# Optimization experiments

Hardware: AMD Instinct MI355X
Metric: run time of the kernel (lower is better)

The kernel has to match this reference:

```python
import jax, jax.numpy as jnp
import numpy as np
import math

DK = 768  # latent_size used for the scale (not the per-head dim, matching the original)

def setup_inputs() -> dict:
    key = jax.random.key(0)
    k1, k2, k3 = jax.random.split(key, 3)
    B, H, S, D = 4, 12, 2048, 64
    queries = jax.random.normal(k1, (B, H, S, D), dtype=jnp.float32)
    keys = jax.random.normal(k2, (B, H, S, D), dtype=jnp.float32)
    values = jax.random.normal(k3, (B, S, H, D), dtype=jnp.float32)  # note [B,S,H,D] layout
    return {"queries": queries, "keys": keys, "values": values}

def reference(queries, keys, values):
    # scores: [B,H,S,S]
    scores = jnp.einsum('bhqd,bhkd->bhqk', queries, keys) / math.sqrt(DK)
    probs = jax.nn.softmax(scores, axis=3)
    v = jnp.transpose(values, (0, 2, 1, 3))  # [B,S,H,D] -> [B,H,S,D]
    return jnp.einsum('bhqk,bhkd->bhqd', probs, v)
```

## Files before the change

### kernel.cpp

```cpp
#include <hip/hip_runtime.h>

#define SQ 2048
#define DH 64
#define NH 12
#define NBH 48
#define QTILE 128
#define KTILE 64
#define NITER (SQ / KTILE)
#define NQT (SQ / QTILE)

typedef short short8 __attribute__((ext_vector_type(8)));
typedef float f32x4  __attribute__((ext_vector_type(4)));
typedef float f32x16 __attribute__((ext_vector_type(16)));
typedef int   i32x4 __attribute__((ext_vector_type(4)));

#define MFMA32(a, b, c) __builtin_amdgcn_mfma_f32_32x32x16_bf16(a, b, c, 0, 0, 0)

typedef __attribute__((address_space(1))) const void* gas_ptr;
typedef __attribute__((address_space(3))) void* las_ptr;

__device__ __forceinline__ void load_lds16(const void* g, void* l) {
    __builtin_amdgcn_global_load_lds((gas_ptr)g, (las_ptr)l, 16, 0, 0);
}

#if defined(__has_builtin) && __has_builtin(__builtin_amdgcn_cvt_pk_bf16_f32)
typedef __bf16 bf16x2_t __attribute__((ext_vector_type(2)));
__device__ __forceinline__ unsigned pk2bf(float a, float b) {
    bf16x2_t v = __builtin_amdgcn_cvt_pk_bf16_f32(a, b);
    union { bf16x2_t v; unsigned u; } c; c.v = v; return c.u;
}
#else
__device__ __forceinline__ unsigned pk2bf(float a, float b) {
    union { float f; unsigned u; } x, y; x.f = a; y.f = b;
    unsigned ra = x.u + 0x7FFFu + ((x.u >> 16) & 1u);
    unsigned rb = y.u + 0x7FFFu + ((y.u >> 16) & 1u);
    return (ra >> 16) | (rb & 0xFFFF0000u);
}
#endif

#define KCONV_BLOCKS (NBH * SQ * DH / 8 / 256)
__global__ __launch_bounds__(256)
void prepass(const float* __restrict__ K, short* __restrict__ Kb,
             const float* __restrict__ V, short* __restrict__ Vt) {
    __shared__ float Ls[64][68];
    if (blockIdx.x < KCONV_BLOCKS) {
        const size_t i = (size_t)(blockIdx.x * 256 + threadIdx.x) * 8;
        f32x4 a = *(const f32x4*)&K[i];
        f32x4 b = *(const f32x4*)&K[i + 4];
        unsigned o[4] = { pk2bf(a[0], a[1]), pk2bf(a[2], a[3]),
                          pk2bf(b[0], b[1]), pk2bf(b[2], b[3]) };
        *(i32x4*)&Kb[i] = *(i32x4*)o;
        return;
    }
    const int bx = blockIdx.x - KCONV_BLOCKS;
    const int st = bx & 31;
    const int bh = bx >> 5;
    const int b = bh / NH, h = bh % NH;
    const int s0 = st * 64;
    const float* src = V + ((size_t)b * SQ * NH + (size_t)h) * DH;
    const int dg = threadIdx.x & 15;
    const int sl = threadIdx.x >> 4;
    #pragma unroll
    for (int p = 0; p < 4; ++p) {
        const int row = p * 16 + sl;
        *(f32x4*)&Ls[row][dg * 4] =
            *(const f32x4*)&src[(size_t)(s0 + row) * (NH * DH) + dg * 4];
    }
    __syncthreads();
    const int dr = threadIdx.x >> 2;
    const int sc = (threadIdx.x & 3) * 16;
    unsigned out[8];
    #pragma unroll
    for (int jj = 0; jj < 8; ++jj)
        out[jj] = pk2bf(Ls[sc + 2 * jj][dr], Ls[sc + 2 * jj + 1][dr]);
    short* dst = Vt + (size_t)bh * DH * SQ + (size_t)dr * SQ + s0 + sc;
    *(i32x4*)(dst)     = *(i32x4*)&out[0];
    *(i32x4*)(dst + 8) = *(i32x4*)&out[4];
}

__global__ __launch_bounds__(256, 3)
void attn_fused_kernel(const float* __restrict__ Q,
                       const short* __restrict__ Kb,
                       const short* __restrict__ Vtg,
                       float* __restrict__ O) {
    __shared__ __align__(16) char L[32768];

    const int tid  = threadIdx.x;
    const int lane = tid & 63;
    const int w    = tid >> 6;
    const int m31  = lane & 31;
    const int hl   = lane >> 5;
    const int l7   = lane & 7;

    const int bx  = blockIdx.x;
    const int xcd = bx & 7;
    const int i96 = bx >> 3;
    const int bh  = xcd * 6 + (i96 % 6);
    const int qt  = i96 / 6;
    const int q0 = qt * QTILE;

    const float* Qb  = Q   + (size_t)bh * SQ * DH;
    const short* Kbh = Kb  + (size_t)bh * SQ * DH;
    const short* Vbh = Vtg + (size_t)bh * DH * SQ;
    float*       Ob  = O   + (size_t)bh * SQ * DH;

    const float qscale = 0.03608439182435161f * 1.4426950408889634f;

    short8 qf[4];
    {
        const int qrow = q0 + 32 * w + m31;
        #pragma unroll
        for (int s = 0; s < 4; ++s) {
            const float* src = Qb + (size_t)qrow * DH + 16 * s + 8 * hl;
            f32x4 qa = *(const f32x4*)src;
            f32x4 qb = *(const f32x4*)(src + 4);
            union { unsigned u[4]; short8 v; } f;
            f.u[0] = pk2bf(qa[0] * qscale, qa[1] * qscale);
            f.u[1] = pk2bf(qa[2] * qscale, qa[3] * qscale);
            f.u[2] = pk2bf(qb[0] * qscale, qb[1] * qscale);
            f.u[3] = pk2bf(qb[2] * qscale, qb[3] * qscale);
            qf[s] = f.v;
        }
    }

    const int gk = (lane & 7) ^ (lane >> 3);
    const int rr = w * 8 + (lane >> 3);
    const short* kg0 = Kbh + (size_t)rr * DH + gk * 8;
    const short* kg1 = kg0 + 32 * DH;
    const short* vg0 = Vbh + (size_t)rr * SQ + gk * 8;
    const short* vg1 = vg0 + 32 * SQ;
    const int wslot = w * 1024;

    int aoff[4];
    #pragma unroll
    for (int s = 0; s < 4; ++s) aoff[s] = m31 * 128 + (((2 * s + hl) ^ l7) * 16);

    f32x16 o0 = {}, o1 = {};
    float lp = 0.f;

    auto issue = [&](int bb) {
        load_lds16(kg0, L + bb + wslot);
        load_lds16(kg1, L + bb + 4096 + wslot);
        load_lds16(vg0, L + bb + 8192 + wslot);
        load_lds16(vg1, L + bb + 12288 + wslot);
        kg0 += KTILE * DH; kg1 += KTILE * DH;
        vg0 += KTILE;      vg1 += KTILE;
    };

    auto softmax_pack = [&](const f32x16& sv, short8* dst) {
        #pragma unroll
        for (int wd = 0; wd < 2; ++wd) {
            float p[8];
            #pragma unroll
            for (int j = 0; j < 8; ++j)
                p[j] = __builtin_amdgcn_exp2f(sv[8 * wd + j]);
            lp += ((p[0] + p[1]) + (p[2] + p[3])) +
                  ((p[4] + p[5]) + (p[6] + p[7]));
            unsigned a0 = pk2bf(p[0], p[1]);
            unsigned a1 = pk2bf(p[2], p[3]);
            unsigned b0 = pk2bf(p[4], p[5]);
            unsigned b1 = pk2bf(p[6], p[7]);
            unsigned r0 = (unsigned)__shfl_xor((int)(hl ? a0 : b0), 32, 64);
            unsigned r1 = (unsigned)__shfl_xor((int)(hl ? a1 : b1), 32, 64);
            union { unsigned u[4]; short8 v; } fr;
            fr.u[0] = hl ? r0 : a0;
            fr.u[1] = hl ? r1 : a1;
            fr.u[2] = hl ? b0 : r0;
            fr.u[3] = hl ? b1 : r1;
            dst[wd] = fr.v;
        }
    };

    auto compute = [&](int bb) {
        f32x16 s0 = {}, s1 = {};
        #pragma unroll
        for (int s = 0; s < 4; ++s) {
            short8 ka0 = *(const short8*)(L + bb + aoff[s]);
            short8 ka1 = *(const short8*)(L + bb + 4096 + aoff[s]);
            s0 = MFMA32(ka0, qf[s], s0);
            s1 = MFMA32(ka1, qf[s], s1);
        }
        short8 pfrag[4];
        softmax_pack(s0, &pfrag[0]);
        softmax_pack(s1, &pfrag[2]);
        #pragma unroll
        for (int s = 0; s < 4; ++s) {
            short8 vb0 = *(const short8*)(L + bb + 8192 + aoff[s]);
            short8 vb1 = *(const short8*)(L + bb + 12288 + aoff[s]);
            o0 = MFMA32(pfrag[s], vb0, o0);
            o1 = MFMA32(pfrag[s], vb1, o1);
        }
    };

    issue(0);
    for (int it = 0; it < NITER; it += 2) {
        __syncthreads();
        issue(16384);
        compute(0);
        __syncthreads();
        if (it + 2 < NITER) issue(0);
        compute(16384);
    }

    float v = lp;
    v += __shfl_xor(v, 32, 64);
    const float linv = 1.0f / v;

    #pragma unroll
    for (int dt = 0; dt < 2; ++dt) {
        const f32x16& o = dt ? o1 : o0;
        #pragma unroll
        for (int reg = 0; reg < 16; ++reg) {
            const int qp = (reg & 3) + 8 * (reg >> 2) + 4 * hl;
            const float rl = __shfl(linv, qp, 64);
            const int q = q0 + 32 * w + qp;
            Ob[(size_t)q * DH + 32 * dt + m31] = o[reg] * rl;
        }
    }
}

extern "C" void kernel_launch(void* const* d_in, const int* in_sizes, int n_in,
                              void* d_out, int out_size, void* d_ws, size_t ws_size,
                              hipStream_t stream) {
    const float* Q = (const float*)d_in[0];
    const float* K = (const float*)d_in[1];
    const float* V = (const float*)d_in[2];
    float* O = (float*)d_out;

    short* Kb  = (short*)d_ws;
    short* Vtg = Kb + (size_t)NBH * SQ * DH;

    prepass<<<dim3(KCONV_BLOCKS + NBH * 32), dim3(256), 0, stream>>>(K, Kb, V, Vtg);
    attn_fused_kernel<<<dim3(NBH * NQT), dim3(256), 0, stream>>>(Q, Kb, Vtg, O);
}
```

Measured before the change: 175.6 us.

## Software-pipeline QK of next tile with softmax and PV of current tile

K and V now get separate double-buffered LDS slots and are issued on their own schedules. The main loop computes QK scores for tile t+1 while running exp/pack and the PV MFMAs for tile t, with one barrier per tile instead of one per half-step. This lets the MFMA work overlap the transcendental softmax work. The cross-half shuffle is replaced by permlane32_swap when the builtin exists, and the row sum is accumulated as a packed float2. The cost is extra registers to hold the next tile's scores, which may reduce occupancy at launch bounds of 3 blocks.

```diff
diff --git a/kernel.cpp b/kernel.cpp
--- a/kernel.cpp
+++ b/kernel.cpp
@@ -10,8 +10,10 @@
 #define NQT (SQ / QTILE)
 
 typedef short short8 __attribute__((ext_vector_type(8)));
+typedef float f32x2  __attribute__((ext_vector_type(2)));
 typedef float f32x4  __attribute__((ext_vector_type(4)));
 typedef float f32x16 __attribute__((ext_vector_type(16)));
+typedef int   i32x2 __attribute__((ext_vector_type(2)));
 typedef int   i32x4 __attribute__((ext_vector_type(4)));
 
 #define MFMA32(a, b, c) __builtin_amdgcn_mfma_f32_32x32x16_bf16(a, b, c, 0, 0, 0)
@@ -36,6 +38,16 @@
     unsigned rb = y.u + 0x7FFFu + ((y.u >> 16) & 1u);
     return (ra >> 16) | (rb & 0xFFFF0000u);
 }
+#endif
+
+#ifdef __has_builtin
+#if __has_builtin(__builtin_amdgcn_permlane32_swap)
+#define HAVE_PLSWAP 1
+#else
+#define HAVE_PLSWAP 0
+#endif
+#else
+#define HAVE_PLSWAP 0
 #endif
 
 #define KCONV_BLOCKS (NBH * SQ * DH / 8 / 256)
@@ -136,15 +148,19 @@
     for (int s = 0; s < 4; ++s) aoff[s] = m31 * 128 + (((2 * s + hl) ^ l7) * 16);
 
     f32x16 o0 = {}, o1 = {};
-    float lp = 0.f;
-
-    auto issue = [&](int bb) {
-        load_lds16(kg0, L + bb + wslot);
-        load_lds16(kg1, L + bb + 4096 + wslot);
-        load_lds16(vg0, L + bb + 8192 + wslot);
-        load_lds16(vg1, L + bb + 12288 + wslot);
-        kg0 += KTILE * DH; kg1 += KTILE * DH;
-        vg0 += KTILE;      vg1 += KTILE;
+    f32x2 lp2 = {0.f, 0.f};
+
+    auto issueK = [&](int slot, int t) {
+        const short* p0 = kg0 + (size_t)t * (KTILE * DH);
+        const short* p1 = kg1 + (size_t)t * (KTILE * DH);
+        load_lds16(p0, L + slot * 8192 + wslot);
+        load_lds16(p1, L + slot * 8192 + 4096 + wslot);
+    };
+    auto issueV = [&](int slot, int t) {
+        const short* p0 = vg0 + (size_t)t * KTILE;
+        const short* p1 = vg1 + (size_t)t * KTILE;
+        load_lds16(p0, L + 16384 + slot * 8192 + wslot);
+        load_lds16(p1, L + 16384 + slot * 8192 + 4096 + wslot);
     };
 
     auto softmax_pack = [&](const f32x16& sv, short8* dst) {
@@ -154,54 +170,77 @@
             #pragma unroll
             for (int j = 0; j < 8; ++j)
                 p[j] = __builtin_amdgcn_exp2f(sv[8 * wd + j]);
-            lp += ((p[0] + p[1]) + (p[2] + p[3])) +
-                  ((p[4] + p[5]) + (p[6] + p[7]));
+            f32x2 s01 = {p[0], p[1]}, s23 = {p[2], p[3]};
+            f32x2 s45 = {p[4], p[5]}, s67 = {p[6], p[7]};
+            lp2 += (s01 + s23) + (s45 + s67);
             unsigned a0 = pk2bf(p[0], p[1]);
             unsigned a1 = pk2bf(p[2], p[3]);
             unsigned b0 = pk2bf(p[4], p[5]);
             unsigned b1 = pk2bf(p[6], p[7]);
+            union { unsigned u[4]; short8 v; } fr;
+#if HAVE_PLSWAP
+            i32x2 r0 = __builtin_amdgcn_permlane32_swap((int)a0, (int)b0, false, false);
+            i32x2 r1 = __builtin_amdgcn_permlane32_swap((int)a1, (int)b1, false, false);
+            fr.u[0] = (unsigned)r0.x;
+            fr.u[1] = (unsigned)r1.x;
+            fr.u[2] = (unsigned)r0.y;
+            fr.u[3] = (unsigned)r1.y;
+#else
             unsigned r0 = (unsigned)__shfl_xor((int)(hl ? a0 : b0), 32, 64);
             unsigned r1 = (unsigned)__shfl_xor((int)(hl ? a1 : b1), 32, 64);
-            union { unsigned u[4]; short8 v; } fr;
             fr.u[0] = hl ? r0 : a0;
             fr.u[1] = hl ? r1 : a1;
             fr.u[2] = hl ? b0 : r0;
             fr.u[3] = hl ? b1 : r1;
+#endif
             dst[wd] = fr.v;
         }
     };
 
-    auto compute = [&](int bb) {
-        f32x16 s0 = {}, s1 = {};
+    auto qk = [&](int slot, f32x16& t0, f32x16& t1) {
+        f32x16 a0 = {}, a1 = {};
         #pragma unroll
         for (int s = 0; s < 4; ++s) {
-            short8 ka0 = *(const short8*)(L + bb + aoff[s]);
-            short8 ka1 = *(const short8*)(L + bb + 4096 + aoff[s]);
-            s0 = MFMA32(ka0, qf[s], s0);
-            s1 = MFMA32(ka1, qf[s], s1);
-        }
-        short8 pfrag[4];
-        softmax_pack(s0, &pfrag[0]);
-        softmax_pack(s1, &pfrag[2]);
+            short8 ka0 = *(const short8*)(L + slot * 8192 + aoff[s]);
+            short8 ka1 = *(const short8*)(L + slot * 8192 + 4096 + aoff[s]);
+            a0 = MFMA32(ka0, qf[s], a0);
+            a1 = MFMA32(ka1, qf[s], a1);
+        }
+        t0 = a0; t1 = a1;
+    };
+
+    auto smpv = [&](int slot, const f32x16& sc0, const f32x16& sc1) {
+        short8 pf[4];
+        softmax_pack(sc0, &pf[0]);
+        softmax_pack(sc1, &pf[2]);
         #pragma unroll
         for (int s = 0; s < 4; ++s) {
-            short8 vb0 = *(const short8*)(L + bb + 8192 + aoff[s]);
-            short8 vb1 = *(const short8*)(L + bb + 12288 + aoff[s]);
-            o0 = MFMA32(pfrag[s], vb0, o0);
-            o1 = MFMA32(pfrag[s], vb1, o1);
-        }
-    };
-
-    issue(0);
-    for (int it = 0; it < NITER; it += 2) {
+            short8 vb0 = *(const short8*)(L + 16384 + slot * 8192 + aoff[s]);
+            short8 vb1 = *(const short8*)(L + 16384 + slot * 8192 + 4096 + aoff[s]);
+            o0 = MFMA32(pf[s], vb0, o0);
+            o1 = MFMA32(pf[s], vb1, o1);
+        }
+    };
+
+    issueK(0, 0); issueV(0, 0); issueK(1, 1);
+    __syncthreads();
+    f32x16 sc0, sc1;
+    qk(0, sc0, sc1);
+
+    #pragma unroll 2
+    for (int t = 0; t < NITER - 1; ++t) {
         __syncthreads();
-        issue(16384);
-        compute(0);
-        __syncthreads();
-        if (it + 2 < NITER) issue(0);
-        compute(16384);
-    }
-
+        if (t + 2 < NITER) issueK(t & 1, t + 2);
+        issueV((t + 1) & 1, t + 1);
+        f32x16 sn0, sn1;
+        qk((t + 1) & 1, sn0, sn1);
+        smpv(t & 1, sc0, sc1);
+        sc0 = sn0; sc1 = sn1;
+    }
+    __syncthreads();
+    smpv((NITER - 1) & 1, sc0, sc1);
+
+    float lp = lp2.x + lp2.y;
     float v = lp;
     v += __shfl_xor(v, 32, 64);
     const float linv = 1.0f / v;
```

Measured after the change: 517.6 us. 2.95x slower.
